# Kernel tuning notes

Measured on AMD Instinct MI355X. Metric: run time of the kernel, lower is better.

Reference implementation:

```python
import jax, jax.numpy as jnp
import numpy as np

CH = 16
R = 9  # reduced_res = ceil(log2(256)+1)


def grid_sample_bilinear(P, gx, gy):
    """torch.F.grid_sample, mode=bilinear, align_corners=True, zeros padding.
    P: (C, H, W); gx indexes width (last axis), gy indexes height. Returns (C, N)."""
    C, H, W = P.shape
    ix = (gx + 1.0) * 0.5 * (W - 1)
    iy = (gy + 1.0) * 0.5 * (H - 1)
    x0 = jnp.floor(ix)
    y0 = jnp.floor(iy)
    wx = ix - x0
    wy = iy - y0
    x0i = jnp.clip(x0.astype(jnp.int32), 0, W - 1)
    x1i = jnp.clip(x0i + 1, 0, W - 1)
    y0i = jnp.clip(y0.astype(jnp.int32), 0, H - 1)
    y1i = jnp.clip(y0i + 1, 0, H - 1)
    v00 = P[:, y0i, x0i]
    v01 = P[:, y0i, x1i]
    v10 = P[:, y1i, x0i]
    v11 = P[:, y1i, x1i]
    return (v00 * (1 - wx) * (1 - wy) + v01 * wx * (1 - wy)
            + v10 * (1 - wx) * wy + v11 * wx * wy)


def plane_feature(P, gx, gy, c_int):
    # sample -> (N, ch, R), then cosine-basis numerical integration over R
    s = grid_sample_bilinear(P, gx, gy)              # (R*ch, N)
    s = s.T.reshape(-1, CH, R)                       # (N, ch, R)
    c = (c_int + 1.0) * 0.5 * (2.0 ** (R - 1) - 1.0)  # (N,)
    freqs = (2.0 ** jnp.arange(R, dtype=jnp.float32)) - 0.5
    basis = jnp.cos(jnp.pi * (c[:, None] + 0.5) * freqs / (2.0 ** R))  # (N, R)
    return 2.0 * jnp.einsum('nr,ncr->nc', basis, s)  # (N, ch)


def setup_inputs() -> dict:
    key = jax.random.key(0)
    k1, k2, k3, k4 = jax.random.split(key, 4)
    coords = jax.random.uniform(k1, (524288, 3), dtype=jnp.float32) * 2.0 - 1.0
    Pu = jax.random.normal(k2, (R * CH, 256, 256), dtype=jnp.float32) * 0.1
    Pv = jax.random.normal(k3, (R * CH, 256, 256), dtype=jnp.float32) * 0.1
    Pw = jax.random.normal(k4, (R * CH, 256, 256), dtype=jnp.float32) * 0.1
    return {"coords": coords, "Pu": Pu, "Pv": Pv, "Pw": Pw}


def reference(coords, Pu, Pv, Pw):
    # Pu sampled with (coord1, coord2), integrated along coord0; etc.
    fu = plane_feature(Pu, coords[:, 1], coords[:, 2], coords[:, 0])
    fv = plane_feature(Pv, coords[:, 0], coords[:, 2], coords[:, 1])
    fw = plane_feature(Pw, coords[:, 0], coords[:, 1], coords[:, 2])
    return fu + fv + fw  # (N, ch)
```

## Files before the change

kernel.cpp:

```cpp
#include <hip/hip_runtime.h>
#include <hip/hip_bf16.h>

#define CHN 16
#define RF 9
#define HWDIM 256
#define POSN (HWDIM * HWDIM)
#define NBINS 32768

typedef _Float16 half2_t __attribute__((ext_vector_type(2)));

__device__ __forceinline__ half2_t u2h(uint32_t u) {
    union { uint32_t u; half2_t h; } x; x.u = u; return x.h;
}
__device__ __forceinline__ uint32_t f2h(float f) {
    union { _Float16 h; uint16_t u; } x; x.h = (_Float16)f; return (uint32_t)x.u;
}
__device__ __forceinline__ float h2f(uint32_t u) {
    union { uint16_t u; _Float16 h; } x; x.u = (uint16_t)u; return (float)x.h;
}

#if __has_builtin(__builtin_amdgcn_fdot2)
__device__ __forceinline__ float DOT2(half2_t a, half2_t b, float c) {
    return __builtin_amdgcn_fdot2(a, b, c, false);
}
#else
__device__ __forceinline__ float DOT2(half2_t a, half2_t b, float c) {
    return fmaf((float)a.x, (float)b.x, fmaf((float)a.y, (float)b.y, c));
}
#endif

__device__ __forceinline__ uint32_t part1by2(uint32_t x) {
    x &= 0x3ffu;
    x = (x | (x << 16)) & 0x030000FFu;
    x = (x | (x << 8))  & 0x0300F00Fu;
    x = (x | (x << 4))  & 0x030C30C3u;
    x = (x | (x << 2))  & 0x09249249u;
    return x;
}
__device__ __forceinline__ uint32_t morton_key(float c0, float c1, float c2) {
    int q0 = min(31, max(0, (int)((c0 + 1.f) * 16.f)));
    int q1 = min(31, max(0, (int)((c1 + 1.f) * 16.f)));
    int q2 = min(31, max(0, (int)((c2 + 1.f) * 16.f)));
    return (part1by2((uint32_t)q0) << 2) | (part1by2((uint32_t)q1) << 1) | part1by2((uint32_t)q2);
}

__device__ __forceinline__ void pack_tile(int tile,
                                          const float* __restrict__ Pu,
                                          const float* __restrict__ Pv,
                                          const float* __restrict__ Pw,
                                          uint4* __restrict__ A,
                                          uint32_t* __restrict__ B,
                                          int t, uint4* LA, uint32_t* LB) {
    int p = tile >> 9;
    int pos_base = (tile & 511) * 128;
    const float* P = (p == 0) ? Pu : ((p == 1) ? Pv : Pw);
    uint32_t r8pk[8];
    const float* Pc0 = P + pos_base + t;
#pragma unroll
    for (int cc = 0; cc < CHN; ++cc) {
        const float* Pc = Pc0 + (size_t)(cc * RF) * POSN;
        uint32_t w[4];
#pragma unroll
        for (int j = 0; j < 4; ++j) {
            float v0 = Pc[(size_t)(2 * j) * POSN];
            float v1 = Pc[(size_t)(2 * j + 1) * POSN];
            w[j] = f2h(v0) | (f2h(v1) << 16);
        }
        LA[t * 17 + cc] = make_uint4(w[0], w[1], w[2], w[3]);
        uint32_t h8 = f2h(Pc[(size_t)8 * POSN]);
        if (cc & 1) r8pk[cc >> 1] |= (h8 << 16); else r8pk[cc >> 1] = h8;
    }
#pragma unroll
    for (int j = 0; j < 8; ++j) LB[t * 9 + j] = r8pk[j];
    __syncthreads();
    uint4* Aout = A + ((size_t)p * POSN + pos_base) * CHN;
#pragma unroll
    for (int it = 0; it < 16; ++it) {
        int i = it * 128 + t;
        Aout[i] = LA[(i >> 4) * 17 + (i & 15)];
    }
    uint32_t* Bout = B + ((size_t)p * POSN + pos_base) * 8;
#pragma unroll
    for (int it = 0; it < 8; ++it) {
        int i = it * 128 + t;
        Bout[i] = LB[(i >> 3) * 9 + (i & 7)];
    }
}

__global__ __launch_bounds__(128) void fuse_hist(const float* __restrict__ Pu,
                                                 const float* __restrict__ Pv,
                                                 const float* __restrict__ Pw,
                                                 uint4* __restrict__ A,
                                                 uint32_t* __restrict__ B,
                                                 const float* __restrict__ coords,
                                                 uint32_t* __restrict__ hist,
                                                 int N, int npack, int tile_lo) {
    __shared__ uint4 LA[128 * 17];
    __shared__ uint32_t LB[128 * 9];
    int b = blockIdx.x, t = threadIdx.x;
    if (b < npack) {
        pack_tile(tile_lo + b, Pu, Pv, Pw, A, B, t, LA, LB);
    } else {
        int n = (b - npack) * 128 + t;
        if (n < N) {
            float c0 = coords[3 * n], c1 = coords[3 * n + 1], c2 = coords[3 * n + 2];
            atomicAdd(&hist[morton_key(c0, c1, c2)], 1u);
        }
    }
}

__global__ __launch_bounds__(128) void fuse_scan(const float* __restrict__ Pu,
                                                 const float* __restrict__ Pv,
                                                 const float* __restrict__ Pw,
                                                 uint4* __restrict__ A,
                                                 uint32_t* __restrict__ B,
                                                 uint32_t* __restrict__ hist,
                                                 int npack, int tile_lo) {
    __shared__ uint4 LA[128 * 17];
    __shared__ uint32_t LB[128 * 9];
    int b = blockIdx.x, t = threadIdx.x;
    if (b == 0) {
        __shared__ uint32_t sh[128];
        const int PER = NBINS / 128;
        int base = t * PER;
        uint32_t s = 0;
        for (int i = 0; i < PER; ++i) s += hist[base + i];
        sh[t] = s;
        __syncthreads();
        for (int off = 1; off < 128; off <<= 1) {
            uint32_t v = (t >= off) ? sh[t - off] : 0u;
            __syncthreads();
            sh[t] += v;
            __syncthreads();
        }
        uint32_t run = sh[t] - s;
        for (int i = 0; i < PER; ++i) {
            uint32_t h = hist[base + i];
            hist[base + i] = run;
            run += h;
        }
    } else {
        pack_tile(tile_lo + (b - 1), Pu, Pv, Pw, A, B, t, LA, LB);
    }
}

__global__ __launch_bounds__(128) void fuse_scatter(const float* __restrict__ Pu,
                                                    const float* __restrict__ Pv,
                                                    const float* __restrict__ Pw,
                                                    uint4* __restrict__ A,
                                                    uint32_t* __restrict__ B,
                                                    const float* __restrict__ coords,
                                                    uint32_t* __restrict__ hist,
                                                    float4* __restrict__ sorted,
                                                    int N, int npack, int tile_lo) {
    __shared__ uint4 LA[128 * 17];
    __shared__ uint32_t LB[128 * 9];
    int b = blockIdx.x, t = threadIdx.x;
    if (b < npack) {
        pack_tile(tile_lo + b, Pu, Pv, Pw, A, B, t, LA, LB);
    } else {
        int n = (b - npack) * 128 + t;
        if (n < N) {
            float c0 = coords[3 * n], c1 = coords[3 * n + 1], c2 = coords[3 * n + 2];
            uint32_t key = morton_key(c0, c1, c2);
            uint32_t dst = atomicAdd(&hist[key], 1u);
            sorted[dst] = make_float4(c0, c1, c2, __uint_as_float((uint32_t)n));
        }
    }
}

__global__ __launch_bounds__(256) void triplane_f16v2(const float4* __restrict__ sorted,
                                                      const uint4* __restrict__ A,
                                                      const uint32_t* __restrict__ B,
                                                      float* __restrict__ out, int N, int nblk) {
    __shared__ float4 pts[32];
    __shared__ uint32_t meta[32 * 40];
    int blk = blockIdx.x;
    {
        int q = nblk >> 3, r = nblk & 7;
        int xcd = blk & 7, local = blk >> 3;
        blk = (xcd < r ? xcd * (q + 1) : r * (q + 1) + (xcd - r) * q) + local;
    }
    int base = blk * 32;
    int t = threadIdx.x;
    if (t < 32) {
        int i = base + t;
        pts[t] = (i < N) ? sorted[i] : make_float4(0.f, 0.f, 0.f, __uint_as_float(0u));
    }
    __syncthreads();
    if (t < 128 && (t & 3) < 3) {
        int pt = t >> 2, p = t & 3;
        float4 c = pts[pt];
        float gx = (p == 0) ? c.y : c.x;
        float gy = (p == 2) ? c.y : c.z;
        float ci = (p == 0) ? c.x : ((p == 1) ? c.y : c.z);
        float ix = (gx + 1.f) * 127.5f;
        float iy = (gy + 1.f) * 127.5f;
        float x0f = floorf(ix), y0f = floorf(iy);
        float wx = ix - x0f, wy = iy - y0f;
        int x0 = min(max((int)x0f, 0), HWDIM - 1);
        int y0 = min(max((int)y0f, 0), HWDIM - 1);
        int x1 = min(x0 + 1, HWDIM - 1);
        int y1 = min(y0 + 1, HWDIM - 1);
        uint32_t* m = &meta[pt * 40 + p * 13];
        float cv = (ci + 1.f) * 127.5f + 0.5f;
        float bb[9];
#pragma unroll
        for (int r = 0; r < 9; ++r) {
            const float k = 3.14159265358979f * ((float)(1 << r) - 0.5f) * (1.f / 512.f);
            bb[r] = __cosf(cv * k);
        }
#pragma unroll
        for (int j = 0; j < 4; ++j) m[j] = f2h(bb[2 * j]) | (f2h(bb[2 * j + 1]) << 16);
        m[4] = __float_as_uint(bb[8]);
        m[5] = __float_as_uint((1.f - wx) * (1.f - wy));
        m[6] = __float_as_uint(wx * (1.f - wy));
        m[7] = __float_as_uint((1.f - wx) * wy);
        m[8] = __float_as_uint(wx * wy);
        m[9]  = (uint32_t)(y0 * HWDIM + x0) * 256u;
        m[10] = (uint32_t)(y0 * HWDIM + x1) * 256u;
        m[11] = (uint32_t)(y1 * HWDIM + x0) * 256u;
        m[12] = (uint32_t)(y1 * HWDIM + x1) * 256u;
    }
    __syncthreads();
    int cc = t & 15, slot = t >> 4;
    const char* Ab = (const char*)A;
    const char* Bb = (const char*)B;
    const uint32_t bofs = ((uint32_t)(cc >> 1) << 2);
    float acc0 = 0.f, acc1 = 0.f;
#pragma unroll
    for (int p = 0; p < 3; ++p) {
        const uint32_t* m0 = &meta[slot * 40 + p * 13];
        const uint32_t* m1 = &meta[(slot + 16) * 40 + p * 13];
        const char* Apl = Ab + (size_t)p * ((size_t)POSN * 256);
        const char* Bpl = Bb + (size_t)p * ((size_t)POSN * 32);
        {
            half2_t b01 = u2h(m0[0]), b23 = u2h(m0[1]), b45 = u2h(m0[2]), b67 = u2h(m0[3]);
            float b8 = __uint_as_float(m0[4]);
#pragma unroll
            for (int k = 0; k < 4; ++k) {
                uint32_t ob = m0[9 + k];
                uint4 a = *(const uint4*)(Apl + ob + cc * 16);
                uint32_t bw = *(const uint32_t*)(Bpl + (ob >> 3) + bofs);
                float v8 = h2f((cc & 1) ? (bw >> 16) : (bw & 0xffffu));
                float s = b8 * v8;
                s = DOT2(u2h(a.x), b01, s);
                s = DOT2(u2h(a.y), b23, s);
                s = DOT2(u2h(a.z), b45, s);
                s = DOT2(u2h(a.w), b67, s);
                acc0 = fmaf(__uint_as_float(m0[5 + k]), s, acc0);
            }
        }
        {
            half2_t b01 = u2h(m1[0]), b23 = u2h(m1[1]), b45 = u2h(m1[2]), b67 = u2h(m1[3]);
            float b8 = __uint_as_float(m1[4]);
#pragma unroll
            for (int k = 0; k < 4; ++k) {
                uint32_t ob = m1[9 + k];
                uint4 a = *(const uint4*)(Apl + ob + cc * 16);
                uint32_t bw = *(const uint32_t*)(Bpl + (ob >> 3) + bofs);
                float v8 = h2f((cc & 1) ? (bw >> 16) : (bw & 0xffffu));
                float s = b8 * v8;
                s = DOT2(u2h(a.x), b01, s);
                s = DOT2(u2h(a.y), b23, s);
                s = DOT2(u2h(a.z), b45, s);
                s = DOT2(u2h(a.w), b67, s);
                acc1 = fmaf(__uint_as_float(m1[5 + k]), s, acc1);
            }
        }
    }
    if (base + slot < N) {
        uint32_t n = __float_as_uint(pts[slot].w);
        out[(size_t)n * CHN + cc] = 2.f * acc0;
    }
    if (base + slot + 16 < N) {
        uint32_t n = __float_as_uint(pts[slot + 16].w);
        out[(size_t)n * CHN + cc] = 2.f * acc1;
    }
}

__global__ __launch_bounds__(256) void triplane_direct(const float* __restrict__ coords,
                                                       const float* __restrict__ Pu,
                                                       const float* __restrict__ Pv,
                                                       const float* __restrict__ Pw,
                                                       float* __restrict__ out, int N) {
    int tid = blockIdx.x * blockDim.x + threadIdx.x;
    int n = tid >> 4;
    if (n >= N) return;
    int cc = tid & 15;
    float c0 = coords[3 * n + 0];
    float c1 = coords[3 * n + 1];
    float c2 = coords[3 * n + 2];
    float acc = 0.f;
#pragma unroll
    for (int p = 0; p < 3; ++p) {
        const float* P = (p == 0) ? Pu : ((p == 1) ? Pv : Pw);
        float gx = (p == 0) ? c1 : c0;
        float gy = (p == 2) ? c1 : c2;
        float ci = (p == 0) ? c0 : ((p == 1) ? c1 : c2);
        float ix = (gx + 1.f) * 127.5f;
        float iy = (gy + 1.f) * 127.5f;
        float x0f = floorf(ix), y0f = floorf(iy);
        float wx = ix - x0f, wy = iy - y0f;
        int x0 = min(max((int)x0f, 0), HWDIM - 1);
        int y0 = min(max((int)y0f, 0), HWDIM - 1);
        int x1 = min(x0 + 1, HWDIM - 1);
        int y1 = min(y0 + 1, HWDIM - 1);
        float cv = (ci + 1.f) * 127.5f + 0.5f;
        float w00 = (1.f - wx) * (1.f - wy), w01 = wx * (1.f - wy);
        float w10 = (1.f - wx) * wy, w11 = wx * wy;
        int p00 = y0 * HWDIM + x0, p01 = y0 * HWDIM + x1;
        int p10 = y1 * HWDIM + x0, p11 = y1 * HWDIM + x1;
#pragma unroll
        for (int r = 0; r < RF; ++r) {
            const float k = 3.14159265358979f * ((float)(1 << r) - 0.5f) / 512.f;
            float b = __cosf(cv * k);
            const float* Pc = P + (size_t)(cc * RF + r) * POSN;
            float v = w00 * Pc[p00] + w01 * Pc[p01] + w10 * Pc[p10] + w11 * Pc[p11];
            acc = fmaf(b, v, acc);
        }
    }
    out[(size_t)n * CHN + cc] = 2.f * acc;
}

extern "C" void kernel_launch(void* const* d_in, const int* in_sizes, int n_in,
                              void* d_out, int out_size, void* d_ws, size_t ws_size,
                              hipStream_t stream) {
    const float* coords = (const float*)d_in[0];
    const float* Pu = (const float*)d_in[1];
    const float* Pv = (const float*)d_in[2];
    const float* Pw = (const float*)d_in[3];
    float* out = (float*)d_out;
    int N = in_sizes[0] / 3;

    size_t offA = 0;
    size_t szA = (size_t)3 * POSN * CHN * sizeof(uint4);
    size_t offB = offA + szA;
    size_t szB = (size_t)3 * POSN * 8 * sizeof(uint32_t);
    size_t offS = offB + szB;
    size_t szS = (size_t)N * sizeof(float4);
    size_t offH = offS + szS;
    size_t szH = (size_t)NBINS * sizeof(uint32_t);
    size_t need = offH + szH;

    if (ws_size >= need) {
        char* ws = (char*)d_ws;
        uint4* A = (uint4*)(ws + offA);
        uint32_t* B = (uint32_t*)(ws + offB);
        float4* sorted = (float4*)(ws + offS);
        uint32_t* hist = (uint32_t*)(ws + offH);

        int tblk = (3 * POSN) / 128;
        int s1 = tblk / 3;
        int s2 = tblk / 3;
        int s3 = tblk - s1 - s2;
        int hblk = (N + 127) / 128;

        hipMemsetAsync(hist, 0, szH, stream);
        fuse_hist<<<s1 + hblk, 128, 0, stream>>>(Pu, Pv, Pw, A, B, coords, hist, N, s1, 0);
        fuse_scan<<<1 + s2, 128, 0, stream>>>(Pu, Pv, Pw, A, B, hist, s2, s1);
        fuse_scatter<<<s3 + hblk, 128, 0, stream>>>(Pu, Pv, Pw, A, B, coords, hist, sorted,
                                                    N, s3, s1 + s2);
        int nblk = (N + 31) / 32;
        triplane_f16v2<<<nblk, 256, 0, stream>>>(sorted, A, B, out, N, nblk);
    } else {
        int threads = N * CHN;
        triplane_direct<<<(threads + 255) / 256, 256, 0, stream>>>(coords, Pu, Pv, Pw, out, N);
    }
}
```

Measured before the change: 200.1 us.

## Pack planes per-channel per thread without LDS transpose; restructure triplane accumulation loop

The plane packing step now gives each thread one (position, channel) pair and writes its uint4 straight to global memory, with no shared-memory staging. The packed B words are combined across neighbouring lanes with a shuffle. This removes the LDS transpose and its barrier and raises block size to 256. The cost is that each global read now covers only 16 positions, so reads are less coalesced. The main sampling kernel also handles its two points one after the other in a loop, each with a per-plane partial sum, which changes register pressure and instruction scheduling.

```diff
diff --git a/kernel.cpp b/kernel.cpp
--- a/kernel.cpp
+++ b/kernel.cpp
@@ -44,50 +44,33 @@
     return (part1by2((uint32_t)q0) << 2) | (part1by2((uint32_t)q1) << 1) | part1by2((uint32_t)q2);
 }
 
-__device__ __forceinline__ void pack_tile(int tile,
-                                          const float* __restrict__ Pu,
-                                          const float* __restrict__ Pv,
-                                          const float* __restrict__ Pw,
-                                          uint4* __restrict__ A,
-                                          uint32_t* __restrict__ B,
-                                          int t, uint4* LA, uint32_t* LB) {
-    int p = tile >> 9;
-    int pos_base = (tile & 511) * 128;
+__device__ __forceinline__ void pack_tile16(int tile,
+                                            const float* __restrict__ Pu,
+                                            const float* __restrict__ Pv,
+                                            const float* __restrict__ Pw,
+                                            uint4* __restrict__ A,
+                                            uint32_t* __restrict__ B, int t) {
+    int p = tile >> 12;
+    int pos = ((tile & 4095) << 4) + (t >> 4);
+    int cc = t & 15;
     const float* P = (p == 0) ? Pu : ((p == 1) ? Pv : Pw);
-    uint32_t r8pk[8];
-    const float* Pc0 = P + pos_base + t;
-#pragma unroll
-    for (int cc = 0; cc < CHN; ++cc) {
-        const float* Pc = Pc0 + (size_t)(cc * RF) * POSN;
-        uint32_t w[4];
-#pragma unroll
-        for (int j = 0; j < 4; ++j) {
-            float v0 = Pc[(size_t)(2 * j) * POSN];
-            float v1 = Pc[(size_t)(2 * j + 1) * POSN];
-            w[j] = f2h(v0) | (f2h(v1) << 16);
-        }
-        LA[t * 17 + cc] = make_uint4(w[0], w[1], w[2], w[3]);
-        uint32_t h8 = f2h(Pc[(size_t)8 * POSN]);
-        if (cc & 1) r8pk[cc >> 1] |= (h8 << 16); else r8pk[cc >> 1] = h8;
-    }
-#pragma unroll
-    for (int j = 0; j < 8; ++j) LB[t * 9 + j] = r8pk[j];
-    __syncthreads();
-    uint4* Aout = A + ((size_t)p * POSN + pos_base) * CHN;
-#pragma unroll
-    for (int it = 0; it < 16; ++it) {
-        int i = it * 128 + t;
-        Aout[i] = LA[(i >> 4) * 17 + (i & 15)];
-    }
-    uint32_t* Bout = B + ((size_t)p * POSN + pos_base) * 8;
-#pragma unroll
-    for (int it = 0; it < 8; ++it) {
-        int i = it * 128 + t;
-        Bout[i] = LB[(i >> 3) * 9 + (i & 7)];
-    }
-}
-
-__global__ __launch_bounds__(128) void fuse_hist(const float* __restrict__ Pu,
+    const float* Pc = P + (size_t)(cc * RF) * POSN + pos;
+    uint32_t w[4];
+#pragma unroll
+    for (int j = 0; j < 4; ++j) {
+        float v0 = Pc[(size_t)(2 * j) * POSN];
+        float v1 = Pc[(size_t)(2 * j + 1) * POSN];
+        w[j] = f2h(v0) | (f2h(v1) << 16);
+    }
+    A[((size_t)p * POSN + pos) * CHN + cc] = make_uint4(w[0], w[1], w[2], w[3]);
+    uint32_t h8 = f2h(Pc[(size_t)8 * POSN]);
+    uint32_t other = __shfl_xor(h8, 1);
+    if (!(cc & 1)) {
+        B[((size_t)p * POSN + pos) * 8 + (cc >> 1)] = h8 | (other << 16);
+    }
+}
+
+__global__ __launch_bounds__(256) void fuse_hist(const float* __restrict__ Pu,
                                                  const float* __restrict__ Pv,
                                                  const float* __restrict__ Pw,
                                                  uint4* __restrict__ A,
@@ -95,13 +78,11 @@
                                                  const float* __restrict__ coords,
                                                  uint32_t* __restrict__ hist,
                                                  int N, int npack, int tile_lo) {
-    __shared__ uint4 LA[128 * 17];
-    __shared__ uint32_t LB[128 * 9];
     int b = blockIdx.x, t = threadIdx.x;
     if (b < npack) {
-        pack_tile(tile_lo + b, Pu, Pv, Pw, A, B, t, LA, LB);
+        pack_tile16(tile_lo + b, Pu, Pv, Pw, A, B, t);
     } else {
-        int n = (b - npack) * 128 + t;
+        int n = (b - npack) * 256 + t;
         if (n < N) {
             float c0 = coords[3 * n], c1 = coords[3 * n + 1], c2 = coords[3 * n + 2];
             atomicAdd(&hist[morton_key(c0, c1, c2)], 1u);
@@ -109,25 +90,23 @@
     }
 }
 
-__global__ __launch_bounds__(128) void fuse_scan(const float* __restrict__ Pu,
+__global__ __launch_bounds__(256) void fuse_scan(const float* __restrict__ Pu,
                                                  const float* __restrict__ Pv,
                                                  const float* __restrict__ Pw,
                                                  uint4* __restrict__ A,
                                                  uint32_t* __restrict__ B,
                                                  uint32_t* __restrict__ hist,
                                                  int npack, int tile_lo) {
-    __shared__ uint4 LA[128 * 17];
-    __shared__ uint32_t LB[128 * 9];
     int b = blockIdx.x, t = threadIdx.x;
     if (b == 0) {
-        __shared__ uint32_t sh[128];
-        const int PER = NBINS / 128;
+        __shared__ uint32_t sh[256];
+        const int PER = NBINS / 256;
         int base = t * PER;
         uint32_t s = 0;
         for (int i = 0; i < PER; ++i) s += hist[base + i];
         sh[t] = s;
         __syncthreads();
-        for (int off = 1; off < 128; off <<= 1) {
+        for (int off = 1; off < 256; off <<= 1) {
             uint32_t v = (t >= off) ? sh[t - off] : 0u;
             __syncthreads();
             sh[t] += v;
@@ -140,11 +119,11 @@
             run += h;
         }
     } else {
-        pack_tile(tile_lo + (b - 1), Pu, Pv, Pw, A, B, t, LA, LB);
-    }
-}
-
-__global__ __launch_bounds__(128) void fuse_scatter(const float* __restrict__ Pu,
+        pack_tile16(tile_lo + (b - 1), Pu, Pv, Pw, A, B, t);
+    }
+}
+
+__global__ __launch_bounds__(256) void fuse_scatter(const float* __restrict__ Pu,
                                                     const float* __restrict__ Pv,
                                                     const float* __restrict__ Pw,
                                                     uint4* __restrict__ A,
@@ -153,13 +132,11 @@
                                                     uint32_t* __restrict__ hist,
                                                     float4* __restrict__ sorted,
                                                     int N, int npack, int tile_lo) {
-    __shared__ uint4 LA[128 * 17];
-    __shared__ uint32_t LB[128 * 9];
     int b = blockIdx.x, t = threadIdx.x;
     if (b < npack) {
-        pack_tile(tile_lo + b, Pu, Pv, Pw, A, B, t, LA, LB);
+        pack_tile16(tile_lo + b, Pu, Pv, Pw, A, B, t);
     } else {
-        int n = (b - npack) * 128 + t;
+        int n = (b - npack) * 256 + t;
         if (n < N) {
             float c0 = coords[3 * n], c1 = coords[3 * n + 1], c2 = coords[3 * n + 2];
             uint32_t key = morton_key(c0, c1, c2);
@@ -227,19 +204,22 @@
     const char* Ab = (const char*)A;
     const char* Bb = (const char*)B;
     const uint32_t bofs = ((uint32_t)(cc >> 1) << 2);
-    float acc0 = 0.f, acc1 = 0.f;
-#pragma unroll
-    for (int p = 0; p < 3; ++p) {
-        const uint32_t* m0 = &meta[slot * 40 + p * 13];
-        const uint32_t* m1 = &meta[(slot + 16) * 40 + p * 13];
-        const char* Apl = Ab + (size_t)p * ((size_t)POSN * 256);
-        const char* Bpl = Bb + (size_t)p * ((size_t)POSN * 32);
-        {
-            half2_t b01 = u2h(m0[0]), b23 = u2h(m0[1]), b45 = u2h(m0[2]), b67 = u2h(m0[3]);
-            float b8 = __uint_as_float(m0[4]);
+#pragma unroll
+    for (int half = 0; half < 2; ++half) {
+        int pt = slot + half * 16;
+        int gi = base + pt;
+        float acc = 0.f;
+#pragma unroll
+        for (int p = 0; p < 3; ++p) {
+            const uint32_t* m = &meta[pt * 40 + p * 13];
+            half2_t b01 = u2h(m[0]), b23 = u2h(m[1]), b45 = u2h(m[2]), b67 = u2h(m[3]);
+            float b8 = __uint_as_float(m[4]);
+            const char* Apl = Ab + (size_t)p * ((size_t)POSN * 256);
+            const char* Bpl = Bb + (size_t)p * ((size_t)POSN * 32);
+            float ps = 0.f;
 #pragma unroll
             for (int k = 0; k < 4; ++k) {
-                uint32_t ob = m0[9 + k];
+                uint32_t ob = m[9 + k];
                 uint4 a = *(const uint4*)(Apl + ob + cc * 16);
                 uint32_t bw = *(const uint32_t*)(Bpl + (ob >> 3) + bofs);
                 float v8 = h2f((cc & 1) ? (bw >> 16) : (bw & 0xffffu));
@@ -248,34 +228,14 @@
                 s = DOT2(u2h(a.y), b23, s);
                 s = DOT2(u2h(a.z), b45, s);
                 s = DOT2(u2h(a.w), b67, s);
-                acc0 = fmaf(__uint_as_float(m0[5 + k]), s, acc0);
+                ps = fmaf(__uint_as_float(m[5 + k]), s, ps);
             }
-        }
-        {
-            half2_t b01 = u2h(m1[0]), b23 = u2h(m1[1]), b45 = u2h(m1[2]), b67 = u2h(m1[3]);
-            float b8 = __uint_as_float(m1[4]);
-#pragma unroll
-            for (int k = 0; k < 4; ++k) {
-                uint32_t ob = m1[9 + k];
-                uint4 a = *(const uint4*)(Apl + ob + cc * 16);
-                uint32_t bw = *(const uint32_t*)(Bpl + (ob >> 3) + bofs);
-                float v8 = h2f((cc & 1) ? (bw >> 16) : (bw & 0xffffu));
-                float s = b8 * v8;
-                s = DOT2(u2h(a.x), b01, s);
-                s = DOT2(u2h(a.y), b23, s);
-                s = DOT2(u2h(a.z), b45, s);
-                s = DOT2(u2h(a.w), b67, s);
-                acc1 = fmaf(__uint_as_float(m1[5 + k]), s, acc1);
-            }
-        }
-    }
-    if (base + slot < N) {
-        uint32_t n = __float_as_uint(pts[slot].w);
-        out[(size_t)n * CHN + cc] = 2.f * acc0;
-    }
-    if (base + slot + 16 < N) {
-        uint32_t n = __float_as_uint(pts[slot + 16].w);
-        out[(size_t)n * CHN + cc] = 2.f * acc1;
+            acc += ps;
+        }
+        if (gi < N) {
+            uint32_t n = __float_as_uint(pts[pt].w);
+            out[(size_t)n * CHN + cc] = 2.f * acc;
+        }
     }
 }
 
@@ -350,16 +310,16 @@
         float4* sorted = (float4*)(ws + offS);
         uint32_t* hist = (uint32_t*)(ws + offH);
 
-        int tblk = (3 * POSN) / 128;
+        int tblk = (3 * POSN) / 16;
         int s1 = tblk / 3;
         int s2 = tblk / 3;
         int s3 = tblk - s1 - s2;
-        int hblk = (N + 127) / 128;
+        int hblk = (N + 255) / 256;
 
         hipMemsetAsync(hist, 0, szH, stream);
-        fuse_hist<<<s1 + hblk, 128, 0, stream>>>(Pu, Pv, Pw, A, B, coords, hist, N, s1, 0);
-        fuse_scan<<<1 + s2, 128, 0, stream>>>(Pu, Pv, Pw, A, B, hist, s2, s1);
-        fuse_scatter<<<s3 + hblk, 128, 0, stream>>>(Pu, Pv, Pw, A, B, coords, hist, sorted,
+        fuse_hist<<<s1 + hblk, 256, 0, stream>>>(Pu, Pv, Pw, A, B, coords, hist, N, s1, 0);
+        fuse_scan<<<1 + s2, 256, 0, stream>>>(Pu, Pv, Pw, A, B, hist, s2, s1);
+        fuse_scatter<<<s3 + hblk, 256, 0, stream>>>(Pu, Pv, Pw, A, B, coords, hist, sorted,
                                                     N, s3, s1 + s2);
         int nblk = (N + 31) / 32;
         triplane_f16v2<<<nblk, 256, 0, stream>>>(sorted, A, B, out, N, nblk);
```

Result: no change. 204.1 us (+2.0%).
